# Performance work log

Measured on AMD Instinct MI355X. Metric: run time of the kernel, lower is better.

## Reference

```python
import jax, jax.numpy as jnp
import numpy as np

N_DOF = 7
HID = 128
BATCH = 65536
EPS_M = 1e-3      # mass-matrix PSD jitter
EPS_B = 1e-3      # friction-matrix PSD jitter
EPS_SOLVE = 1e-4  # jitter added before linalg.solve
N_CHOL = N_DOF * (N_DOF + 1) // 2  # 28
TRI_I, TRI_J = np.tril_indices(N_DOF)
DIAG_MASK = jnp.asarray(TRI_I == TRI_J)


def _mlp(x, p):
    # p = (W0,b0,W1,b1,W2,b2,W3,b3): Linear+Softplus x3 then Linear (n_layers=3)
    W0, b0, W1, b1, W2, b2, W3, b3 = p
    h = jax.nn.softplus(x @ W0 + b0)
    h = jax.nn.softplus(h @ W1 + b1)
    h = jax.nn.softplus(h @ W2 + b2)
    return h @ W3 + b3


def _psd(chol_vec, eps):
    # chol_vec: (n_chol,) lower-triangular entries row-major (i, j<=i); exp on diagonal
    vals = jnp.where(DIAG_MASK, jnp.exp(chol_vec), chol_vec)
    L = jnp.zeros((N_DOF, N_DOF), chol_vec.dtype).at[TRI_I, TRI_J].set(vals)
    return L @ L.T + eps * jnp.eye(N_DOF, dtype=chol_vec.dtype)


def _accel_single(q, qd, mp, pp, fp):
    mass = lambda qq: _psd(_mlp(qq, mp), EPS_M)

    def lagrangian(qq, qdd):
        M = mass(qq)
        V = jax.nn.softplus(_mlp(qq, pp))[0]
        return 0.5 * qdd @ (M @ qdd) - V

    dL_dq = jax.grad(lagrangian, argnums=0)(q, qd)
    # L is quadratic in qdot => Hessian wrt qdot (M_rows loop in torch) is exactly M(q)
    M = mass(q)
    # Coriolis_i = (d/dq [M(q) qd]_i) . qd  == jvp of q -> M(q) qd in direction qd
    _, coriolis = jax.jvp(lambda qq: mass(qq) @ qd, (q,), (qd,))
    B_mat = _psd(_mlp(q, fp), EPS_B)
    friction = B_mat @ qd
    rhs = dL_dq - coriolis - friction
    return jnp.linalg.solve(M + EPS_SOLVE * jnp.eye(N_DOF, dtype=q.dtype), rhs)


def setup_inputs() -> dict:
    key = jax.random.key(0)
    keys = iter(jax.random.split(key, 64))

    def lin(fan_in, fan_out):
        W = jax.random.normal(next(keys), (fan_in, fan_out), jnp.float32) / np.sqrt(fan_in)
        b = jax.random.normal(next(keys), (fan_out,), jnp.float32) * 0.01
        return W, b

    inp = {
        "q": jax.random.normal(next(keys), (BATCH, N_DOF), jnp.float32),
        "qdot": jax.random.normal(next(keys), (BATCH, N_DOF), jnp.float32),
    }
    for name, out_dim in [("m", N_CHOL), ("p", 1), ("f", N_CHOL)]:
        dims = [(N_DOF, HID), (HID, HID), (HID, HID), (HID, out_dim)]
        for li, (fi, fo) in enumerate(dims):
            W, b = lin(fi, fo)
            inp[f"{name}W{li}"] = W
            inp[f"{name}b{li}"] = b
    return inp


def reference(q, qdot,
              mW0, mb0, mW1, mb1, mW2, mb2, mW3, mb3,
              pW0, pb0, pW1, pb1, pW2, pb2, pW3, pb3,
              fW0, fb0, fW1, fb1, fW2, fb2, fW3, fb3):
    mp = (mW0, mb0, mW1, mb1, mW2, mb2, mW3, mb3)
    pp = (pW0, pb0, pW1, pb1, pW2, pb2, pW3, pb3)
    fp = (fW0, fb0, fW1, fb1, fW2, fb2, fW3, fb3)
    return jax.vmap(_accel_single, in_axes=(0, 0, None, None, None))(q, qdot, mp, pp, fp)
```

## Files before the change

### kernel.cpp

```cpp
#include <hip/hip_runtime.h>

#define NT 512
#define TM 32
#define NBLK (65536/TM)

typedef unsigned int u32;
typedef unsigned short u16;
typedef __attribute__((ext_vector_type(4))) float f32x4;
typedef __attribute__((ext_vector_type(8))) _Float16 f16x8;
typedef __attribute__((ext_vector_type(4))) _Float16 f16x4;

namespace {
constexpr int TI_[28] = {0,1,1,2,2,2,3,3,3,3,4,4,4,4,4,5,5,5,5,5,5,6,6,6,6,6,6,6};
constexpr int TJ_[28] = {0,0,1,0,1,2,0,1,2,3,0,1,2,3,4,0,1,2,3,4,5,0,1,2,3,4,5,6};
constexpr bool DG_[28] = {1,0,1,0,0,1,0,0,0,1,0,0,0,0,1,0,0,0,0,0,1,0,0,0,0,0,0,1};

constexpr int IB[20] = {0,16384,81920,147456,163840,180224,245760,311296,319488,
                        335872,401408,466944,475136,540672,606208,614400,630784,
                        696320,761856,778240};
constexpr int IN_[19]  = {128,128,128,32,128,128,128,16,128,128,128,16,128,128,16,128,128,128,32};
constexpr int ITY_[19] = {0,1,1,2,3,4,4,5,0,1,1,6,4,4,5,0,1,1,2};
constexpr int TOTF16 = 778240/2;
}

__device__ __forceinline__ float sp_f(float z) {
  float t = exp2f(-fabsf(z)*1.44269504f);
  return fmaxf(z, 0.f) + 0.69314718f*__log2f(1.f + t);
}
__device__ __forceinline__ float sigm_f(float z) {
  float t = exp2f(-z*1.44269504f);
  return __builtin_amdgcn_rcpf(1.f + t);
}
__device__ __forceinline__ float sig_a(float a) {
  return 1.f - exp2f(-a*1.44269504f);
}

__device__ __forceinline__ u16 h2b(_Float16 h) { union{_Float16 f; u16 u;} c; c.f = h; return c.u; }
__device__ __forceinline__ u16 f16b(float x)   { return h2b((_Float16)x); }
__device__ __forceinline__ float b2f(u16 b)    { union{u16 u; _Float16 f;} c; c.u = b; return (float)c.f; }
__device__ __forceinline__ f16x8 fz8()         { return (f16x8)(_Float16)0.f; }

__device__ __forceinline__ f32x4 mm(f16x8 a, f16x8 b, f32x4 c) {
  return __builtin_amdgcn_mfma_f32_16x16x32_f16(a, b, c, 0, 0, 0);
}

__device__ __forceinline__ f16x8 aread(const u16* P, int row, int s) {
  return *(const f16x8*)(P + row*128 + ((s ^ (row & 7)) << 3));
}
__device__ __forceinline__ int aidx4(int mrow, int n2) {
  return mrow*128 + (((n2 >> 3) ^ (mrow & 7)) << 3) + (n2 & 7);
}
__device__ __forceinline__ void awrite4(u16* P, int mrow, int n2, f16x4 v) {
  *(f16x4*)(P + aidx4(mrow, n2)) = v;
}
__device__ __forceinline__ f16x4 aread4(const u16* P, int mrow, int n2) {
  return *(const f16x4*)(P + aidx4(mrow, n2));
}
__device__ __forceinline__ f16x8 aq8(const u16* P, int row, int g) {
  f16x8 v = *(const f16x8*)(P + row*8);
  return g ? fz8() : v;
}
__device__ __forceinline__ f16x8 ubread(const u16* P, int row, int g) {
  return *(const f16x8*)(P + row*32 + ((g ^ (row & 3)) << 3));
}
__device__ __forceinline__ f16x8 bread(const char* img, int N, int sk, int n) {
  return *(const f16x8*)(img + ((sk*N + n) << 4));
}

struct __align__(16) Smem {
  u16 mh1[4096], mh2[4096], mh3[4096];
  u16 X[4096], Y[4096];
  u16 qmh[256], qml[256], qdb[256];
  u16 ub[1024];
  float cTm[896];
  u16 dcH[896], cfH[896];
  float GQ1[256], GQp[256];
  float V[32];
};
static_assert(sizeof(Smem) <= 54613, "need 3 blocks/CU");

template<int KS, bool QSRC, int TC>
__device__ __forceinline__ void fwd_hl(const u16* Bh, const u16* Bl, u16* Oh, u16* Ol,
                                       const char* img, int hb, const float* bias,
                                       int tile0, int tstep, int l) {
  const int m = l & 15, g = l >> 4;
  f32x4 H[TC][2], X[TC][2];
  #pragma unroll
  for (int j=0;j<TC;++j)
    #pragma unroll
    for (int mt=0;mt<2;++mt) { H[j][mt]=(f32x4){0,0,0,0}; X[j][mt]=(f32x4){0,0,0,0}; }
  #pragma unroll
  for (int ks=0; ks<KS; ++ks) {
    const int sk = ks*4 + g;
    f16x8 bh[2], bl[2];
    #pragma unroll
    for (int mt=0;mt<2;++mt) {
      const int row = mt*16+m;
      bh[mt] = QSRC ? aq8(Bh,row,g) : aread(Bh,row,sk);
      bl[mt] = QSRC ? aq8(Bl,row,g) : aread(Bl,row,sk);
    }
    #pragma unroll
    for (int j=0;j<TC;++j) {
      const int n = (tile0 + j*tstep)*16 + m;
      const f16x8 wh = bread(img,128,sk,n);
      const f16x8 wl = bread(img+hb,128,sk,n);
      #pragma unroll
      for (int mt=0;mt<2;++mt) {
        H[j][mt]=mm(wh,bh[mt],H[j][mt]);
        X[j][mt]=mm(wl,bh[mt],X[j][mt]);
        X[j][mt]=mm(wh,bl[mt],X[j][mt]);
      }
    }
  }
  #pragma unroll
  for (int j=0;j<TC;++j) {
    const int n2 = (tile0 + j*tstep)*16 + 4*g;
    f32x4 bv = bias ? *(const f32x4*)(bias + n2) : (f32x4){0,0,0,0};
    #pragma unroll
    for (int mt=0;mt<2;++mt) {
      const int mrow = mt*16 + m;
      f16x4 vh, vl;
      #pragma unroll
      for (int r=0;r<4;++r) {
        const float o = sp_f(H[j][mt][r] + X[j][mt][r]*(1.f/4096.f) + bv[r]);
        const _Float16 hh = (_Float16)o;
        vh[r] = hh;
        vl[r] = (_Float16)((o - (float)hh)*4096.f);
      }
      awrite4(Oh, mrow, n2, vh);
      awrite4(Ol, mrow, n2, vl);
    }
  }
}

template<int KS, bool QSRC, int TC>
__device__ __forceinline__ void fwd_h(const u16* Bh, u16* Oh, const char* img,
                                      const float* bias, int tile0, int tstep, int l) {
  const int m = l & 15, g = l >> 4;
  f32x4 H[TC][2];
  #pragma unroll
  for (int j=0;j<TC;++j)
    #pragma unroll
    for (int mt=0;mt<2;++mt) H[j][mt]=(f32x4){0,0,0,0};
  #pragma unroll
  for (int ks=0; ks<KS; ++ks) {
    const int sk = ks*4 + g;
    f16x8 bh[2];
    #pragma unroll
    for (int mt=0;mt<2;++mt) {
      const int row = mt*16+m;
      bh[mt] = QSRC ? aq8(Bh,row,g) : aread(Bh,row,sk);
    }
    #pragma unroll
    for (int j=0;j<TC;++j) {
      const f16x8 wh = bread(img,128,sk,(tile0 + j*tstep)*16+m);
      #pragma unroll
      for (int mt=0;mt<2;++mt) H[j][mt]=mm(wh,bh[mt],H[j][mt]);
    }
  }
  #pragma unroll
  for (int j=0;j<TC;++j) {
    const int n2 = (tile0 + j*tstep)*16 + 4*g;
    f32x4 bv = bias ? *(const f32x4*)(bias + n2) : (f32x4){0,0,0,0};
    #pragma unroll
    for (int mt=0;mt<2;++mt) {
      const int mrow = mt*16 + m;
      f16x4 vh;
      #pragma unroll
      for (int r=0;r<4;++r) vh[r] = (_Float16)sp_f(H[j][mt][r] + bv[r]);
      awrite4(Oh, mrow, n2, vh);
    }
  }
}

template<int TC>
__device__ __forceinline__ void grad128(const u16* Bin, const u16* Sig, u16* Out,
                                        const char* img, int tile0, int tstep, int l) {
  const int m = l & 15, g = l >> 4;
  f32x4 acc[TC][2];
  #pragma unroll
  for (int j=0;j<TC;++j)
    #pragma unroll
    for (int mt=0;mt<2;++mt) acc[j][mt]=(f32x4){0,0,0,0};
  #pragma unroll
  for (int ks=0; ks<4; ++ks) {
    const int sk = ks*4 + g;
    f16x8 bh[2];
    #pragma unroll
    for (int mt=0;mt<2;++mt) bh[mt] = aread(Bin, mt*16+m, sk);
    #pragma unroll
    for (int j=0;j<TC;++j) {
      const f16x8 wh = bread(img,128,sk,(tile0 + j*tstep)*16+m);
      #pragma unroll
      for (int mt=0;mt<2;++mt) acc[j][mt]=mm(wh,bh[mt],acc[j][mt]);
    }
  }
  #pragma unroll
  for (int j=0;j<TC;++j) {
    const int n2 = (tile0 + j*tstep)*16 + 4*g;
    #pragma unroll
    for (int mt=0;mt<2;++mt) {
      const int mrow = mt*16 + m;
      const f16x4 sg = aread4(Sig, mrow, n2);
      f16x4 o;
      #pragma unroll
      for (int r=0;r<4;++r) o[r] = (_Float16)(sig_a((float)sg[r]) * acc[j][mt][r]);
      awrite4(Out, mrow, n2, o);
    }
  }
}

template<int ASRC, int TC>
__device__ __forceinline__ void grad32(const u16* Bin, const u16* Sig, u16* Out,
                                       const char* img, int tile0, int tstep, int l) {
  const int m = l & 15, g = l >> 4;
  f32x4 acc[TC][2];
  #pragma unroll
  for (int j=0;j<TC;++j)
    #pragma unroll
    for (int mt=0;mt<2;++mt) acc[j][mt]=(f32x4){0,0,0,0};
  {
    f16x8 bh[2];
    #pragma unroll
    for (int mt=0;mt<2;++mt) {
      const int row = mt*16+m;
      bh[mt] = (ASRC==0) ? ubread(Bin,row,g) : aq8(Bin,row,g);
    }
    #pragma unroll
    for (int j=0;j<TC;++j) {
      const f16x8 wh = bread(img,128,g,(tile0 + j*tstep)*16+m);
      #pragma unroll
      for (int mt=0;mt<2;++mt) acc[j][mt]=mm(wh,bh[mt],acc[j][mt]);
    }
  }
  #pragma unroll
  for (int j=0;j<TC;++j) {
    const int n2 = (tile0 + j*tstep)*16 + 4*g;
    #pragma unroll
    for (int mt=0;mt<2;++mt) {
      const int mrow = mt*16 + m;
      const f16x4 sg = aread4(Sig, mrow, n2);
      f16x4 o;
      #pragma unroll
      for (int r=0;r<4;++r) o[r] = (_Float16)(sig_a((float)sg[r]) * acc[j][mt][r]);
      awrite4(Out, mrow, n2, o);
    }
  }
}

template<int TC>
__device__ __forceinline__ void gradPotF(const u16* A3p, const float* V, float pb3v,
                                         const u16* Sig, u16* Out, const char* img,
                                         int tile0, int tstep, int l) {
  const int m = l & 15, g = l >> 4;
  float up[2];
  #pragma unroll
  for (int mt=0;mt<2;++mt) up[mt] = sigm_f(V[mt*16+m] + pb3v);
  f32x4 acc[TC][2];
  #pragma unroll
  for (int j=0;j<TC;++j)
    #pragma unroll
    for (int mt=0;mt<2;++mt) acc[j][mt]=(f32x4){0,0,0,0};
  #pragma unroll
  for (int ks=0; ks<4; ++ks) {
    const int sk = ks*4 + g;
    f16x8 bh[2];
    #pragma unroll
    for (int mt=0;mt<2;++mt) {
      const f16x8 a3 = aread(A3p, mt*16+m, sk);
      f16x8 t;
      #pragma unroll
      for (int e=0;e<8;++e) t[e] = (_Float16)(up[mt]*sig_a((float)a3[e]));
      bh[mt] = t;
    }
    #pragma unroll
    for (int j=0;j<TC;++j) {
      const f16x8 wh = bread(img,128,sk,(tile0 + j*tstep)*16+m);
      #pragma unroll
      for (int mt=0;mt<2;++mt) acc[j][mt]=mm(wh,bh[mt],acc[j][mt]);
    }
  }
  #pragma unroll
  for (int j=0;j<TC;++j) {
    const int n2 = (tile0 + j*tstep)*16 + 4*g;
    #pragma unroll
    for (int mt=0;mt<2;++mt) {
      const int mrow = mt*16 + m;
      const f16x4 sg = aread4(Sig, mrow, n2);
      f16x4 o;
      #pragma unroll
      for (int r=0;r<4;++r) o[r] = (_Float16)(sig_a((float)sg[r]) * acc[j][mt][r]);
      awrite4(Out, mrow, n2, o);
    }
  }
}

template<bool HL>
__device__ __forceinline__ void l3(const u16* Bh, const u16* Bl, const char* img, int hb,
                                   const float* b3, float* cT, u16* cH, int wg, int l) {
  const int m = l & 15, g = l >> 4;
  const int n2t = wg & 1, mt = wg >> 1;
  const int mrow = mt*16 + m;
  f32x4 H = {0,0,0,0}, X = {0,0,0,0};
  #pragma unroll
  for (int ks=0; ks<4; ++ks) {
    const int sk = ks*4 + g;
    const f16x8 bh = aread(Bh, mrow, sk);
    const f16x8 wh = bread(img,32,sk, n2t*16+m);
    H = mm(wh, bh, H);
    if (HL) {
      const f16x8 wl = bread(img+hb,32,sk, n2t*16+m);
      const f16x8 bl = aread(Bl, mrow, sk);
      X = mm(wl, bh, X);
      X = mm(wh, bl, X);
    }
  }
  const int u0 = n2t*16 + 4*g;
  if (u0 < 28) {
    f32x4 bv = b3 ? *(const f32x4*)(b3 + u0) : (f32x4){0,0,0,0};
    #pragma unroll
    for (int r=0;r<4;++r) {
      const float v = H[r] + (HL ? X[r]*(1.f/4096.f) : 0.f) + bv[r];
      if (HL) cT[(u0+r)*32 + mrow] = v;
      else    cH[(u0+r)*32 + mrow] = f16b(v);
    }
  }
}

template<bool HEAD>
__device__ __forceinline__ void n16(const u16* Bin, const char* img,
                                    float* GQ, float* V, int mt, int l) {
  const int m = l & 15, g = l >> 4;
  const int mrow = mt*16 + m;
  f32x4 acc = {0,0,0,0};
  #pragma unroll
  for (int ks=0; ks<4; ++ks) {
    const int sk = ks*4 + g;
    const f16x8 bh = aread(Bin, mrow, sk);
    const f16x8 wh = bread(img,16,sk,m);
    acc = mm(wh, bh, acc);
  }
  if (HEAD) {
    if (g == 0) V[mrow] = acc[0];
  } else {
    if (g < 2) {
      #pragma unroll
      for (int r=0;r<4;++r) GQ[mrow*8 + 4*g + r] = acc[r];
    }
  }
}

__global__ __launch_bounds__(256)
void pack_kernel(const float* __restrict__ mW0, const float* __restrict__ mb0,
                 const float* __restrict__ mW1, const float* __restrict__ mW2,
                 const float* __restrict__ mW3,
                 const float* __restrict__ pW0, const float* __restrict__ pb0,
                 const float* __restrict__ pW1, const float* __restrict__ pW2,
                 const float* __restrict__ pW3,
                 const float* __restrict__ fW0, const float* __restrict__ fb0,
                 const float* __restrict__ fW1, const float* __restrict__ fW2,
                 const float* __restrict__ fW3,
                 u16* __restrict__ ws)
{
  const int idx = blockIdx.x*256 + threadIdx.x;
  if (idx >= TOTF16) return;
  int img = 0;
  #pragma unroll
  for (int i = 1; i < 19; ++i) if (idx >= IB[i]/2) img = i;
  const int rem = idx - IB[img]/2;
  const int N = IN_[img];
  const int psz = (IB[img+1] - IB[img]) / 4;
  const int plane = rem >= psz;
  const int e = plane ? rem - psz : rem;
  const int slot = e / (N*8);
  const int r1 = e - slot*(N*8);
  const int n = r1 >> 3, ee = r1 & 7;
  const int k = slot*8 + ee;

  const float* W = nullptr; const float* B = nullptr;
  switch (img) {
    case 0:  W = mW0; B = mb0; break;
    case 1:  W = mW1; break;   case 2:  W = mW2; break;
    case 3:  W = mW3; break;   case 4:  W = mW3; break;
    case 5:  W = mW2; break;   case 6:  W = mW1; break;
    case 7:  W = mW0; break;
    case 8:  W = pW0; B = pb0; break;
    case 9:  W = pW1; break;   case 10: W = pW2; break;
    case 11: W = pW3; break;   case 12: W = pW2; break;
    case 13: W = pW1; break;   case 14: W = pW0; break;
    case 15: W = fW0; B = fb0; break;
    case 16: W = fW1; break;   case 17: W = fW2; break;
    default: W = fW3; break;
  }
  float v = 0.f;
  switch (ITY_[img]) {
    case 0: v = (k < 7) ? W[k*128 + n] : (k == 7 ? B[n] : 0.f); break;
    case 1: v = W[k*128 + n]; break;
    case 2: v = (n < 28) ? W[k*28 + n] : 0.f; break;
    case 3: v = (k < 28) ? W[n*28 + k] : 0.f; break;
    case 4: v = W[n*128 + k]; break;
    case 5: v = (n < 7) ? W[n*128 + k] : 0.f; break;
    default: v = (n == 0) ? W[k] : 0.f; break;
  }
  if (img == 12) v *= pW3[k];
  const _Float16 h = (_Float16)v;
  union { _Float16 f; u16 u; } c;
  c.f = plane ? (_Float16)((v - (float)h) * 4096.f) : h;
  ws[idx] = c.u;
}

__global__ __launch_bounds__(NT, 6)
void delan_kernel(const float* __restrict__ qg, const float* __restrict__ qdg,
    const float* __restrict__ mb1, const float* __restrict__ mb2, const float* __restrict__ mb3,
    const float* __restrict__ pb1, const float* __restrict__ pb2, const float* __restrict__ pb3,
    const float* __restrict__ fb1, const float* __restrict__ fb2, const float* __restrict__ fb3,
    const char* __restrict__ ws, float* __restrict__ out)
{
  __shared__ Smem S;
  const int t = threadIdx.x;
  const int l = t & 63;
  const int w = __builtin_amdgcn_readfirstlane(t >> 6);
  const int wg = w & 3;
  const int s0 = blockIdx.x * TM;

  if (t < 256) {
    const int m = t >> 3, c = t & 7;
    const float v = (c < 7) ? qg[(s0 + m)*7 + c] : 1.f;
    const _Float16 hh = (_Float16)v;
    S.qmh[t] = h2b(hh);
    S.qml[t] = f16b((v - (float)hh)*4096.f);
  } else {
    const int idx = t - 256;
    const int m = idx >> 3, c = idx & 7;
    S.qdb[idx] = (c < 7) ? f16b(qdg[(s0 + m)*7 + c]) : (u16)0;
  }
  __syncthreads();

  fwd_hl<1,true,1>(S.qmh, S.qml, S.mh1, S.X, ws+IB[0], (IB[1]-IB[0])/2, nullptr, w, 1, l);
  __syncthreads();
  fwd_hl<4,false,1>(S.mh1, S.X, S.mh2, S.Y, ws+IB[1], (IB[2]-IB[1])/2, mb1, w, 1, l);
  __syncthreads();
  fwd_hl<4,false,1>(S.mh2, S.Y, S.mh3, S.X, ws+IB[2], (IB[3]-IB[2])/2, mb2, w, 1, l);
  __syncthreads();
  if (w < 4) l3<true>(S.mh3, S.X, ws+IB[3], (IB[4]-IB[3])/2, mb3, S.cTm, nullptr, wg, l);
  else       grad32<1,2>(S.qdb, S.mh1, S.Y, ws+IB[0], wg, 4, l);
  __syncthreads();
  if (w == 0 && l < 32) {
    const int ml = l;
    float qdv[7];
    #pragma unroll
    for (int i = 0; i < 7; ++i) qdv[i] = qdg[(s0 + ml)*7 + i];
    float vals[28], wvv[7] = {0,0,0,0,0,0,0};
    #pragma unroll
    for (int u = 0; u < 28; ++u) {
      const float cv = S.cTm[u*32 + ml];
      vals[u] = DG_[u] ? __expf(cv) : cv;
    }
    #pragma unroll
    for (int u = 0; u < 28; ++u) wvv[TJ_[u]] = fmaf(vals[u], qdv[TI_[u]], wvv[TJ_[u]]);
    #pragma unroll
    for (int u = 0; u < 28; ++u) S.cTm[u*32 + ml] = vals[u];
    #pragma unroll
    for (int u = 0; u < 28; ++u) {
      const float uval = (DG_[u] ? vals[u] : 1.f) * qdv[TI_[u]] * wvv[TJ_[u]];
      S.ub[ml*32 + (((u >> 3) ^ (ml & 3)) << 3) + (u & 7)] = f16b(uval);
    }
    #pragma unroll
    for (int u = 28; u < 32; ++u)
      S.ub[ml*32 + (((u >> 3) ^ (ml & 3)) << 3) + (u & 7)] = 0;
  } else if (w >= 4) {
    grad128<2>(S.Y, S.mh2, S.X, ws+IB[1], wg, 4, l);
  }
  __syncthreads();
  grad128<1>(S.X, S.mh3, S.Y, ws+IB[2], w, 1, l);
  __syncthreads();
  if (w < 4) l3<false>(S.Y, nullptr, ws+IB[3], 0, nullptr, nullptr, S.dcH, wg, l);
  else       grad32<0,2>(S.ub, S.mh3, S.X, ws+IB[4], wg, 4, l);
  __syncthreads();
  grad128<1>(S.X, S.mh2, S.Y, ws+IB[5], w, 1, l);
  __syncthreads();
  grad128<1>(S.Y, S.mh1, S.X, ws+IB[6], w, 1, l);
  __syncthreads();
  if (w < 2)       n16<false>(S.X, ws+IB[7], S.GQ1, nullptr, w, l);
  else if (w >= 4) fwd_h<1,true,2>(S.qmh, S.mh1, ws+IB[8], nullptr, wg, 4, l);
  __syncthreads();
  if (w < 4) fwd_h<4,false,2>(S.mh1, S.mh2, ws+IB[9], pb1, wg, 4, l);
  else       fwd_h<1,true,2>(S.qmh, S.Y, ws+IB[15], nullptr, wg, 4, l);
  __syncthreads();
  if (w < 4) fwd_h<4,false,2>(S.mh2, S.mh3, ws+IB[10], pb2, wg, 4, l);
  else       fwd_h<4,false,2>(S.Y, S.X, ws+IB[16], fb1, wg, 4, l);
  __syncthreads();
  if (w < 2)       n16<true>(S.mh3, ws+IB[11], nullptr, S.V, w, l);
  else if (w >= 4) fwd_h<4,false,2>(S.X, S.Y, ws+IB[17], fb2, wg, 4, l);
  __syncthreads();
  if (w < 4) gradPotF<2>(S.mh3, S.V, pb3[0], S.mh2, S.mh2, ws+IB[12], wg, 4, l);
  else       l3<false>(S.Y, nullptr, ws+IB[18], 0, fb3, nullptr, S.cfH, wg, l);
  __syncthreads();
  grad128<1>(S.mh2, S.mh1, S.X, ws+IB[13], w, 1, l);
  __syncthreads();
  if (w < 2) n16<false>(S.X, ws+IB[14], S.GQp, nullptr, w, l);
  __syncthreads();

  if (w == 0 && l < 32) {
    const int ml = l;
    float qdv[7];
    #pragma unroll
    for (int i = 0; i < 7; ++i) qdv[i] = qdg[(s0 + ml)*7 + i];
    float lv[28];
    #pragma unroll
    for (int u = 0; u < 28; ++u) lv[u] = S.cTm[u*32 + ml];
    float wvv[7] = {0,0,0,0,0,0,0};
    #pragma unroll
    for (int u = 0; u < 28; ++u) wvv[TJ_[u]] = fmaf(lv[u], qdv[TI_[u]], wvv[TJ_[u]]);
    float cor[7] = {0,0,0,0,0,0,0}, t2[7] = {0,0,0,0,0,0,0};
    #pragma unroll
    for (int u = 0; u < 28; ++u) {
      const float dv = (DG_[u] ? lv[u] : 1.f) * b2f(S.dcH[u*32 + ml]);
      cor[TI_[u]] = fmaf(dv, wvv[TJ_[u]], cor[TI_[u]]);
      t2[TJ_[u]]  = fmaf(dv, qdv[TI_[u]], t2[TJ_[u]]);
    }
    #pragma unroll
    for (int u = 0; u < 28; ++u) cor[TI_[u]] = fmaf(lv[u], t2[TJ_[u]], cor[TI_[u]]);
    float r7[7];
    #pragma unroll
    for (int i = 0; i < 7; ++i)
      r7[i] = S.GQ1[ml*8 + i] - cor[i] - S.GQp[ml*8 + i] - 1e-3f*qdv[i];
    float fv[28];
    #pragma unroll
    for (int u = 0; u < 28; ++u) {
      const float cv = b2f(S.cfH[u*32 + ml]);
      fv[u] = DG_[u] ? __expf(cv) : cv;
    }
    float wf[7] = {0,0,0,0,0,0,0};
    #pragma unroll
    for (int u = 0; u < 28; ++u) wf[TJ_[u]] = fmaf(fv[u], qdv[TI_[u]], wf[TJ_[u]]);
    #pragma unroll
    for (int u = 0; u < 28; ++u) r7[TI_[u]] -= fv[u]*wf[TJ_[u]];

    float L[7][7];
    #pragma unroll
    for (int i = 0; i < 7; ++i)
      #pragma unroll
      for (int j = 0; j < 7; ++j) L[i][j] = 0.f;
    #pragma unroll
    for (int u = 0; u < 28; ++u) L[TI_[u]][TJ_[u]] = lv[u];

    float M[7][7];
    #pragma unroll
    for (int i = 0; i < 7; ++i)
      #pragma unroll
      for (int j = 0; j < 7; ++j)
        if (j <= i) {
          float sum = (i == j) ? 1.1e-3f : 0.f;
          #pragma unroll
          for (int k = 0; k < 7; ++k) if (k <= j) sum = fmaf(L[i][k], L[j][k], sum);
          M[i][j] = sum;
        }
    float C[7][7];
    #pragma unroll
    for (int i = 0; i < 7; ++i)
      #pragma unroll
      for (int j = 0; j < 7; ++j)
        if (j <= i) {
          float sum = M[i][j];
          #pragma unroll
          for (int k = 0; k < 7; ++k) if (k < j) sum -= C[i][k] * C[j][k];
          if (j == i) C[i][j] = sqrtf(fmaxf(sum, 1e-12f));
          else        C[i][j] = sum / C[j][j];
        }
    float y[7];
    #pragma unroll
    for (int i = 0; i < 7; ++i) {
      float sum = r7[i];
      #pragma unroll
      for (int k = 0; k < 7; ++k) if (k < i) sum -= C[i][k] * y[k];
      y[i] = sum / C[i][i];
    }
    float x[7];
    #pragma unroll
    for (int i = 6; i >= 0; --i) {
      float sum = y[i];
      #pragma unroll
      for (int k = 0; k < 7; ++k) if (k > i) sum -= C[k][i] * x[k];
      x[i] = sum / C[i][i];
    }
    #pragma unroll
    for (int i = 0; i < 7; ++i) out[(s0 + ml)*7 + i] = x[i];
  }
}

extern "C" void kernel_launch(void* const* d_in, const int* in_sizes, int n_in,
                              void* d_out, int out_size, void* d_ws, size_t ws_size,
                              hipStream_t stream) {
  (void)in_sizes; (void)n_in; (void)out_size; (void)ws_size;
  const float* q   = (const float*)d_in[0];
  const float* qd  = (const float*)d_in[1];
  const float* mW0 = (const float*)d_in[2];  const float* mb0 = (const float*)d_in[3];
  const float* mW1 = (const float*)d_in[4];  const float* mb1 = (const float*)d_in[5];
  const float* mW2 = (const float*)d_in[6];  const float* mb2 = (const float*)d_in[7];
  const float* mW3 = (const float*)d_in[8];  const float* mb3 = (const float*)d_in[9];
  const float* pW0 = (const float*)d_in[10]; const float* pb0 = (const float*)d_in[11];
  const float* pW1 = (const float*)d_in[12]; const float* pb1 = (const float*)d_in[13];
  const float* pW2 = (const float*)d_in[14]; const float* pb2 = (const float*)d_in[15];
  const float* pW3 = (const float*)d_in[16]; const float* pb3 = (const float*)d_in[17];
  const float* fW0 = (const float*)d_in[18]; const float* fb0 = (const float*)d_in[19];
  const float* fW1 = (const float*)d_in[20]; const float* fb1 = (const float*)d_in[21];
  const float* fW2 = (const float*)d_in[22]; const float* fb2 = (const float*)d_in[23];
  const float* fW3 = (const float*)d_in[24]; const float* fb3 = (const float*)d_in[25];
  float* out = (float*)d_out;
  u16* ws = (u16*)d_ws;

  pack_kernel<<<dim3((TOTF16 + 255)/256), dim3(256), 0, stream>>>(
      mW0, mb0, mW1, mW2, mW3, pW0, pb0, pW1, pW2, pW3, fW0, fb0, fW1, fW2, fW3, ws);

  delan_kernel<<<dim3(NBLK), dim3(NT), 0, stream>>>(
      q, qd, mb1, mb2, mb3, pb1, pb2, pb3, fb1, fb2, fb3,
      (const char*)ws, out);
}
```

Before: 123.7 us.

## Shrink LDS to fit 3 blocks/CU, add MFMA priority and packed f16 conversion

Aliases the friction Cholesky output buffer onto the ub scratch buffer, so the shared-memory struct fits under the allocation-granule limit and three blocks can stay resident per CU. Wraps the MFMA loops in s_setprio raises so matrix work is favoured during issue. Replaces per-element f16 casts with packed round-toward-zero conversions. The rounding mode changes from nearest-even to toward-zero, and aliasing ub assumes it is no longer live when cfH is written.

```diff
diff --git a/kernel.cpp b/kernel.cpp
--- a/kernel.cpp
+++ b/kernel.cpp
@@ -9,6 +9,7 @@
 typedef __attribute__((ext_vector_type(4))) float f32x4;
 typedef __attribute__((ext_vector_type(8))) _Float16 f16x8;
 typedef __attribute__((ext_vector_type(4))) _Float16 f16x4;
+typedef __attribute__((ext_vector_type(2))) __fp16 fp16x2r;
 
 namespace {
 constexpr int TI_[28] = {0,1,1,2,2,2,3,3,3,3,4,4,4,4,4,5,5,5,5,5,5,6,6,6,6,6,6,6};
@@ -40,6 +41,13 @@
 __device__ __forceinline__ float b2f(u16 b)    { union{u16 u; _Float16 f;} c; c.u = b; return (float)c.f; }
 __device__ __forceinline__ f16x8 fz8()         { return (f16x8)(_Float16)0.f; }
 
+__device__ __forceinline__ f16x4 pk4(f32x4 v) {
+  union { struct { fp16x2r a, b; } p; f16x4 v; } u;
+  u.p.a = __builtin_amdgcn_cvt_pkrtz(v[0], v[1]);
+  u.p.b = __builtin_amdgcn_cvt_pkrtz(v[2], v[3]);
+  return u.v;
+}
+
 __device__ __forceinline__ f32x4 mm(f16x8 a, f16x8 b, f32x4 c) {
   return __builtin_amdgcn_mfma_f32_16x16x32_f16(a, b, c, 0, 0, 0);
 }
@@ -73,11 +81,11 @@
   u16 qmh[256], qml[256], qdb[256];
   u16 ub[1024];
   float cTm[896];
-  u16 dcH[896], cfH[896];
+  u16 dcH[896];
   float GQ1[256], GQp[256];
   float V[32];
 };
-static_assert(sizeof(Smem) <= 54613, "need 3 blocks/CU");
+static_assert(sizeof(Smem) <= 53248, "need 3 blocks/CU incl. alloc granule");
 
 template<int KS, bool QSRC, int TC>
 __device__ __forceinline__ void fwd_hl(const u16* Bh, const u16* Bl, u16* Oh, u16* Ol,
@@ -89,6 +97,7 @@
   for (int j=0;j<TC;++j)
     #pragma unroll
     for (int mt=0;mt<2;++mt) { H[j][mt]=(f32x4){0,0,0,0}; X[j][mt]=(f32x4){0,0,0,0}; }
+  __builtin_amdgcn_s_setprio(1);
   #pragma unroll
   for (int ks=0; ks<KS; ++ks) {
     const int sk = ks*4 + g;
@@ -112,6 +121,7 @@
       }
     }
   }
+  __builtin_amdgcn_s_setprio(0);
   #pragma unroll
   for (int j=0;j<TC;++j) {
     const int n2 = (tile0 + j*tstep)*16 + 4*g;
@@ -142,6 +152,7 @@
   for (int j=0;j<TC;++j)
     #pragma unroll
     for (int mt=0;mt<2;++mt) H[j][mt]=(f32x4){0,0,0,0};
+  __builtin_amdgcn_s_setprio(1);
   #pragma unroll
   for (int ks=0; ks<KS; ++ks) {
     const int sk = ks*4 + g;
@@ -158,6 +169,7 @@
       for (int mt=0;mt<2;++mt) H[j][mt]=mm(wh,bh[mt],H[j][mt]);
     }
   }
+  __builtin_amdgcn_s_setprio(0);
   #pragma unroll
   for (int j=0;j<TC;++j) {
     const int n2 = (tile0 + j*tstep)*16 + 4*g;
@@ -165,10 +177,10 @@
     #pragma unroll
     for (int mt=0;mt<2;++mt) {
       const int mrow = mt*16 + m;
-      f16x4 vh;
-      #pragma unroll
-      for (int r=0;r<4;++r) vh[r] = (_Float16)sp_f(H[j][mt][r] + bv[r]);
-      awrite4(Oh, mrow, n2, vh);
+      f32x4 o;
+      #pragma unroll
+      for (int r=0;r<4;++r) o[r] = sp_f(H[j][mt][r] + bv[r]);
+      awrite4(Oh, mrow, n2, pk4(o));
     }
   }
 }
@@ -182,6 +194,7 @@
   for (int j=0;j<TC;++j)
     #pragma unroll
     for (int mt=0;mt<2;++mt) acc[j][mt]=(f32x4){0,0,0,0};
+  __builtin_amdgcn_s_setprio(1);
   #pragma unroll
   for (int ks=0; ks<4; ++ks) {
     const int sk = ks*4 + g;
@@ -195,6 +208,7 @@
       for (int mt=0;mt<2;++mt) acc[j][mt]=mm(wh,bh[mt],acc[j][mt]);
     }
   }
+  __builtin_amdgcn_s_setprio(0);
   #pragma unroll
   for (int j=0;j<TC;++j) {
     const int n2 = (tile0 + j*tstep)*16 + 4*g;
@@ -202,10 +216,10 @@
     for (int mt=0;mt<2;++mt) {
       const int mrow = mt*16 + m;
       const f16x4 sg = aread4(Sig, mrow, n2);
-      f16x4 o;
-      #pragma unroll
-      for (int r=0;r<4;++r) o[r] = (_Float16)(sig_a((float)sg[r]) * acc[j][mt][r]);
-      awrite4(Out, mrow, n2, o);
+      f32x4 o;
+      #pragma unroll
+      for (int r=0;r<4;++r) o[r] = sig_a((float)sg[r]) * acc[j][mt][r];
+      awrite4(Out, mrow, n2, pk4(o));
     }
   }
 }
@@ -219,6 +233,7 @@
   for (int j=0;j<TC;++j)
     #pragma unroll
     for (int mt=0;mt<2;++mt) acc[j][mt]=(f32x4){0,0,0,0};
+  __builtin_amdgcn_s_setprio(1);
   {
     f16x8 bh[2];
     #pragma unroll
@@ -233,6 +248,7 @@
       for (int mt=0;mt<2;++mt) acc[j][mt]=mm(wh,bh[mt],acc[j][mt]);
     }
   }
+  __builtin_amdgcn_s_setprio(0);
   #pragma unroll
   for (int j=0;j<TC;++j) {
     const int n2 = (tile0 + j*tstep)*16 + 4*g;
@@ -240,10 +256,10 @@
     for (int mt=0;mt<2;++mt) {
       const int mrow = mt*16 + m;
       const f16x4 sg = aread4(Sig, mrow, n2);
-      f16x4 o;
-      #pragma unroll
-      for (int r=0;r<4;++r) o[r] = (_Float16)(sig_a((float)sg[r]) * acc[j][mt][r]);
-      awrite4(Out, mrow, n2, o);
+      f32x4 o;
+      #pragma unroll
+      for (int r=0;r<4;++r) o[r] = sig_a((float)sg[r]) * acc[j][mt][r];
+      awrite4(Out, mrow, n2, pk4(o));
     }
   }
 }
@@ -287,10 +303,10 @@
     for (int mt=0;mt<2;++mt) {
       const int mrow = mt*16 + m;
       const f16x4 sg = aread4(Sig, mrow, n2);
-      f16x4 o;
-      #pragma unroll
-      for (int r=0;r<4;++r) o[r] = (_Float16)(sig_a((float)sg[r]) * acc[j][mt][r]);
-      awrite4(Out, mrow, n2, o);
+      f32x4 o;
+      #pragma unroll
+      for (int r=0;r<4;++r) o[r] = sig_a((float)sg[r]) * acc[j][mt][r];
+      awrite4(Out, mrow, n2, pk4(o));
     }
   }
 }
@@ -302,6 +318,7 @@
   const int n2t = wg & 1, mt = wg >> 1;
   const int mrow = mt*16 + m;
   f32x4 H = {0,0,0,0}, X = {0,0,0,0};
+  __builtin_amdgcn_s_setprio(1);
   #pragma unroll
   for (int ks=0; ks<4; ++ks) {
     const int sk = ks*4 + g;
@@ -315,6 +332,7 @@
       X = mm(wh, bl, X);
     }
   }
+  __builtin_amdgcn_s_setprio(0);
   const int u0 = n2t*16 + 4*g;
   if (u0 < 28) {
     f32x4 bv = b3 ? *(const f32x4*)(b3 + u0) : (f32x4){0,0,0,0};
@@ -422,6 +440,7 @@
   const int w = __builtin_amdgcn_readfirstlane(t >> 6);
   const int wg = w & 3;
   const int s0 = blockIdx.x * TM;
+  u16* const cfH = S.ub;
 
   if (t < 256) {
     const int m = t >> 3, c = t & 7;
@@ -494,7 +513,7 @@
   else if (w >= 4) fwd_h<4,false,2>(S.X, S.Y, ws+IB[17], fb2, wg, 4, l);
   __syncthreads();
   if (w < 4) gradPotF<2>(S.mh3, S.V, pb3[0], S.mh2, S.mh2, ws+IB[12], wg, 4, l);
-  else       l3<false>(S.Y, nullptr, ws+IB[18], 0, fb3, nullptr, S.cfH, wg, l);
+  else       l3<false>(S.Y, nullptr, ws+IB[18], 0, fb3, nullptr, cfH, wg, l);
   __syncthreads();
   grad128<1>(S.mh2, S.mh1, S.X, ws+IB[13], w, 1, l);
   __syncthreads();
@@ -528,7 +547,7 @@
     float fv[28];
     #pragma unroll
     for (int u = 0; u < 28; ++u) {
-      const float cv = b2f(S.cfH[u*32 + ml]);
+      const float cv = b2f(cfH[u*32 + ml]);
       fv[u] = DG_[u] ? __expf(cv) : cv;
     }
     float wf[7] = {0,0,0,0,0,0,0};
```

New measurement: 109.9 us. 11.1% less time.
